# Kernel optimization log

Hardware: AMD Instinct MI355X
Metric: run time of the kernel (lower is better)

Reference implementation:

```python
import jax, jax.numpy as jnp
import numpy as np

N_NODES = 100000
N_EDGES = 1600000
N_FEAT = 128
N_HID = 128
N_CLASS = 10
N_GRAPHS = 512
BN_EPS = 1e-5


def setup_inputs() -> dict:
    key = jax.random.key(0)
    ks = jax.random.split(key, 12)
    x = jax.random.normal(ks[0], (N_NODES, N_FEAT), dtype=jnp.float32)
    edge_index = jax.random.randint(ks[1], (2, N_EDGES), 0, N_NODES, dtype=jnp.int32)
    batch = jnp.sort(jax.random.randint(ks[2], (N_NODES,), 0, N_GRAPHS, dtype=jnp.int32))
    s1 = 1.0 / np.sqrt(N_FEAT)
    s2 = 1.0 / np.sqrt(N_HID)
    W1 = jax.random.uniform(ks[3], (N_FEAT, N_HID), jnp.float32, -s1, s1)
    b1 = jax.random.uniform(ks[4], (N_HID,), jnp.float32, -s1, s1)
    gamma = jnp.ones((N_HID,), jnp.float32)
    beta = jnp.zeros((N_HID,), jnp.float32)
    W2 = jax.random.uniform(ks[5], (N_HID, N_HID), jnp.float32, -s2, s2)
    b2 = jax.random.uniform(ks[6], (N_HID,), jnp.float32, -s2, s2)
    clsW = jax.random.uniform(ks[7], (N_HID, N_CLASS), jnp.float32, -s2, s2)
    clsb = jax.random.uniform(ks[8], (N_CLASS,), jnp.float32, -s2, s2)
    return {"x": x, "edge_index": edge_index, "batch": batch,
            "W1": W1, "b1": b1, "gamma": gamma, "beta": beta,
            "W2": W2, "b2": b2, "clsW": clsW, "clsb": clsb}


def _gcn_norm(edge_index, n_nodes):
    # add self-loops, compute symmetric normalization D^-1/2 A_hat D^-1/2
    loops = jnp.arange(n_nodes, dtype=edge_index.dtype)
    src = jnp.concatenate([edge_index[0], loops])
    dst = jnp.concatenate([edge_index[1], loops])
    deg = jax.ops.segment_sum(jnp.ones_like(dst, dtype=jnp.float32), dst,
                              num_segments=n_nodes)
    dinv = jnp.where(deg > 0, jax.lax.rsqrt(deg), 0.0)
    norm = dinv[src] * dinv[dst]  # [E + N]
    return src, dst, norm


def _gcn_conv(h, src, dst, norm, W, b, n_nodes):
    h = h @ W                                   # [N, nhid] dense GEMM
    msg = h[src] * norm[:, None]                # gather + scale  [E+N, nhid]
    out = jax.ops.segment_sum(msg, dst, num_segments=n_nodes)  # scatter-add
    return out + b


def reference(x, edge_index, batch, W1, b1, gamma, beta, W2, b2, clsW, clsb):
    n_nodes = x.shape[0]
    src, dst, norm = _gcn_norm(edge_index, n_nodes)
    # layer 1: GCNConv -> BatchNorm(eval, running stats 0/1) -> ReLU -> Dropout(eval=id)
    h = _gcn_conv(x, src, dst, norm, W1, b1, n_nodes)
    h = h * (gamma / jnp.sqrt(1.0 + BN_EPS)) + beta
    h = jax.nn.relu(h)
    # layer 2: GCNConv (output layer, no bn/act)
    h = _gcn_conv(h, src, dst, norm, W2, b2, n_nodes)
    # global mean pool over batch index
    sums = jax.ops.segment_sum(h, batch, num_segments=N_GRAPHS)          # [G, nhid]
    cnts = jax.ops.segment_sum(jnp.ones((n_nodes,), h.dtype), batch,
                               num_segments=N_GRAPHS)
    g = sums / jnp.maximum(cnts, 1.0)[:, None]
    out = jax.nn.log_softmax(g @ clsW + clsb, axis=1)                    # [G, nclass]
    return out, g
```

## Files before the change

### kernel.cpp

```cpp
#include <hip/hip_runtime.h>
#include <hip/hip_bf16.h>

#define N_NODES 100000
#define N_EDGES 1600000
#define N_FEAT 128
#define N_HID 128
#define N_CLASS 10
#define N_GRAPHS 512
#define BN_RSQRT 0.9999950000374997f

#define NRANGE 12500
#define NSUB 512
#define SCAP 640
#define HGROUP 32
#define BPB (NSUB / HGROUP)

typedef _Float16 half_t;
typedef __attribute__((ext_vector_type(2))) _Float16 half2v;
typedef __attribute__((ext_vector_type(4))) _Float16 half4v;
typedef __attribute__((ext_vector_type(8))) _Float16 half8v;
typedef __attribute__((ext_vector_type(4))) float floatx4;
typedef __attribute__((ext_vector_type(2))) float floatx2;

__global__ __launch_bounds__(256) void bucket_fused(
    const int* __restrict__ src, const int* __restrict__ dst,
    int* __restrict__ cnt, unsigned long long* __restrict__ bucketed,
    const float* __restrict__ W1, half_t* __restrict__ Wt1,
    const float* __restrict__ W2, half_t* __restrict__ Wt2,
    const int* __restrict__ batch, int* __restrict__ boffs,
    int chunkE, int E, int nnodes)
{
    __shared__ int wcnt[4][8];
    __shared__ int wbase[4][8];
    int blk = blockIdx.x;
    if (blk >= NSUB) {
        int k = blk - NSUB;
        if (k < 128) {
            int i = k * 256 + threadIdx.x;
            const float* W = (i < 16384) ? W1 : W2;
            half_t* Wt = (i < 16384) ? Wt1 : Wt2;
            int j = i & 16383;
            int c = j >> 7, kk = j & 127;
            Wt[(size_t)c * 128 + kk] = (half_t)W[(size_t)kk * 128 + c];
        } else {
            int i = (k - 128) * 256 + threadIdx.x;
            if (i < nnodes) {
                int b = batch[i];
                int prev = (i == 0) ? -1 : batch[i - 1];
                for (int g = prev + 1; g <= b; ++g) boffs[g] = i;
                if (i == nnodes - 1)
                    for (int g = b + 1; g <= N_GRAPHS; ++g) boffs[g] = nnodes;
            }
        }
        return;
    }
    int b = blk;
    int wave = threadIdx.x >> 6;
    int lane = threadIdx.x & 63;
    int e0 = b * chunkE;
    int e1 = e0 + chunkE < E ? e0 + chunkE : E;
    int iters = (chunkE + 255) / 256;

    int mycnt = 0;
    for (int it = 0; it < iters; ++it) {
        int e = e0 + it * 256 + threadIdx.x;
        bool valid = e < e1;
        int d = valid ? dst[e] : 0;
        int rr = (d * 8) / N_NODES;
#pragma unroll
        for (int r = 0; r < 8; ++r) {
            unsigned long long m = __ballot(valid && rr == r);
            if (lane == r) mycnt += __popcll(m);
        }
    }
    if (lane < 8) wcnt[wave][lane] = mycnt;
    __syncthreads();
    if (threadIdx.x < 8) {
        int r = threadIdx.x;
        int s = 0;
#pragma unroll
        for (int w = 0; w < 4; ++w) { wbase[w][r] = s; s += wcnt[w][r]; }
        cnt[r * NSUB + b] = s;
    }
    __syncthreads();

    int myoff = (lane < 8) ? wbase[wave][lane] : 0;
    for (int it = 0; it < iters; ++it) {
        int e = e0 + it * 256 + threadIdx.x;
        bool valid = e < e1;
        int s = valid ? src[e] : 0;
        int d = valid ? dst[e] : 0;
        int rr = (d * 8) / N_NODES;
        unsigned long long pk = ((unsigned long long)(unsigned)d << 32) | (unsigned)s;
#pragma unroll
        for (int r = 0; r < 8; ++r) {
            unsigned long long m = __ballot(valid && rr == r);
            int base_r = __shfl(myoff, r);
            if (valid && rr == r) {
                int pos = base_r + __popcll(m & ((1ull << lane) - 1));
                if (pos < SCAP)
                    bucketed[(size_t)(r * NSUB + b) * SCAP + pos] = pk;
            }
            if (lane == r) myoff += __popcll(m);
        }
    }
}

__global__ __launch_bounds__(256) void hist2(
    const unsigned long long* __restrict__ bucketed, const int* __restrict__ cnt,
    int* __restrict__ partial)
{
    __shared__ int h[NRANGE];
    int r = blockIdx.x & 7, g = blockIdx.x >> 3;
    for (int i = threadIdx.x; i < NRANGE; i += 256) h[i] = 0;
    __syncthreads();
    int rbase = r * NRANGE;
    for (int j = 0; j < BPB; ++j) {
        int b = g * BPB + j;
        int n = cnt[r * NSUB + b];
        if (n > SCAP) n = SCAP;
        const unsigned long long* seg = bucketed + (size_t)(r * NSUB + b) * SCAP;
        for (int i = threadIdx.x; i < n; i += 256)
            atomicAdd(&h[(int)(seg[i] >> 32) - rbase], 1);
    }
    __syncthreads();
    int* slice = partial + (size_t)(r * HGROUP + g) * NRANGE;
    for (int i = threadIdx.x; i < NRANGE; i += 256) slice[i] = h[i];
}

__global__ void deg_reduce(const int* __restrict__ partial, int* __restrict__ deg,
                           float* __restrict__ dinv, int* __restrict__ bsums, int n) {
    __shared__ int sm[256];
    int t = threadIdx.x;
    int i = blockIdx.x * 256 + t;
    int s = 0;
    if (i < n) {
        int rr = i / NRANGE;
        int dl = i - rr * NRANGE;
        const int* p = partial + (size_t)rr * HGROUP * NRANGE + dl;
#pragma unroll 8
        for (int g = 0; g < HGROUP; ++g) s += p[(size_t)g * NRANGE];
        deg[i] = s;
        dinv[i] = rsqrtf((float)s + 1.0f);
    }
    sm[t] = s;
    __syncthreads();
    for (int off = 128; off > 0; off >>= 1) {
        if (t < off) sm[t] += sm[t + off];
        __syncthreads();
    }
    if (t == 0) bsums[blockIdx.x] = sm[0];
}

__global__ void scan_small(int* __restrict__ bsums, int nb) {
    __shared__ int buf[1024];
    int t = threadIdx.x;
    int v = (t < nb) ? bsums[t] : 0;
    buf[t] = v;
    __syncthreads();
    for (int off = 1; off < 1024; off <<= 1) {
        int x = (t >= off) ? buf[t - off] : 0;
        __syncthreads();
        buf[t] += x;
        __syncthreads();
    }
    if (t < nb) bsums[t] = buf[t] - v;
}

__global__ __launch_bounds__(256) void scan_chunkoff_gemm1(
    const int* __restrict__ in, const int* __restrict__ bsums,
    int* __restrict__ rowptr, int* __restrict__ partial,
    int n, int total, int nb,
    const float* __restrict__ X, const half_t* __restrict__ Wt,
    const float* __restrict__ dinv, unsigned char* __restrict__ Y8, int nrows)
{
    __shared__ int s[256];
    if (blockIdx.x < (unsigned)nb) {
        int t = threadIdx.x;
        int i = blockIdx.x * 256 + t;
        int v = (i < n) ? in[i] : 0;
        s[t] = v;
        __syncthreads();
        for (int off = 1; off < 256; off <<= 1) {
            int x = (t >= off) ? s[t - off] : 0;
            __syncthreads();
            s[t] += x;
            __syncthreads();
        }
        if (i == 0) rowptr[n] = total;
        if (i < n) {
            int excl = bsums[blockIdx.x] + s[t] - v;
            rowptr[i] = excl;
            int rr = i / NRANGE;
            int dl = i - rr * NRANGE;
            int* p = partial + (size_t)rr * HGROUP * NRANGE + dl;
            int running = excl;
            for (int g = 0; g < HGROUP; ++g) {
                int tmp = p[(size_t)g * NRANGE];
                p[(size_t)g * NRANGE] = running;
                running += tmp;
            }
        }
        return;
    }
    int bb = blockIdx.x - nb;
    int wave = threadIdx.x >> 6;
    int lane = threadIdx.x & 63;
    int n16  = lane & 15;
    int quad = lane >> 4;
    int r0 = bb * 64 + wave * 16;
    if (r0 >= nrows) return;
    int row = r0 + n16;
    const float4* xrow = (const float4*)(X + (size_t)row * 128);
    half8v a[4];
#pragma unroll
    for (int kc = 0; kc < 4; ++kc) {
        float4 f0 = xrow[kc * 8 + quad * 2];
        float4 f1 = xrow[kc * 8 + quad * 2 + 1];
        half8v t = {(half_t)f0.x, (half_t)f0.y, (half_t)f0.z, (half_t)f0.w,
                    (half_t)f1.x, (half_t)f1.y, (half_t)f1.z, (half_t)f1.w};
        a[kc] = t;
    }
    float dr = dinv[row];
#pragma unroll
    for (int c = 0; c < 8; ++c) {
        const half8v* wrow = (const half8v*)(Wt + (size_t)(c * 16 + n16) * 128);
        floatx4 acc = {0.f, 0.f, 0.f, 0.f};
        acc = __builtin_amdgcn_mfma_f32_16x16x32_f16(wrow[0 * 4 + quad], a[0], acc, 0, 0, 0);
        acc = __builtin_amdgcn_mfma_f32_16x16x32_f16(wrow[1 * 4 + quad], a[1], acc, 0, 0, 0);
        acc = __builtin_amdgcn_mfma_f32_16x16x32_f16(wrow[2 * 4 + quad], a[2], acc, 0, 0, 0);
        acc = __builtin_amdgcn_mfma_f32_16x16x32_f16(wrow[3 * 4 + quad], a[3], acc, 0, 0, 0);
        int packed = __builtin_amdgcn_cvt_pk_fp8_f32(acc[0] * dr, acc[1] * dr, 0, false);
        packed = __builtin_amdgcn_cvt_pk_fp8_f32(acc[2] * dr, acc[3] * dr, packed, true);
        *(int*)(Y8 + (size_t)row * 128 + c * 16 + quad * 4) = packed;
    }
}

__global__ __launch_bounds__(256) void fill2(
    const unsigned long long* __restrict__ bucketed, const int* __restrict__ cnt,
    const int* __restrict__ partial, int* __restrict__ col)
{
    __shared__ int off[NRANGE];
    int r = blockIdx.x & 7, g = blockIdx.x >> 3;
    const int* slice = partial + (size_t)(r * HGROUP + g) * NRANGE;
    for (int i = threadIdx.x; i < NRANGE; i += 256) off[i] = slice[i];
    __syncthreads();
    int rbase = r * NRANGE;
    for (int j = 0; j < BPB; ++j) {
        int b = g * BPB + j;
        int n = cnt[r * NSUB + b];
        if (n > SCAP) n = SCAP;
        const unsigned long long* seg = bucketed + (size_t)(r * NSUB + b) * SCAP;
        for (int i = threadIdx.x; i < n; i += 256) {
            unsigned long long pk = seg[i];
            int pos = atomicAdd(&off[(int)(pk >> 32) - rbase], 1);
            col[pos] = (int)((unsigned)(pk & 0xffffffffu) << 7);
        }
    }
}

__global__ __launch_bounds__(256) void gemm2_mfma(
    const half_t* __restrict__ X, const half_t* __restrict__ Wt,
    const float* __restrict__ dinv, unsigned char* __restrict__ Y8, int nrows)
{
    int wave = threadIdx.x >> 6;
    int lane = threadIdx.x & 63;
    int n16  = lane & 15;
    int quad = lane >> 4;
    int r0 = blockIdx.x * 64 + wave * 16;
    if (r0 >= nrows) return;
    int row = r0 + n16;
    const half8v* xrow = (const half8v*)(X + (size_t)row * 128);
    half8v a0 = xrow[0 * 4 + quad];
    half8v a1 = xrow[1 * 4 + quad];
    half8v a2 = xrow[2 * 4 + quad];
    half8v a3 = xrow[3 * 4 + quad];
    float dr = dinv[row];
#pragma unroll
    for (int c = 0; c < 8; ++c) {
        const half8v* wrow = (const half8v*)(Wt + (size_t)(c * 16 + n16) * 128);
        floatx4 acc = {0.f, 0.f, 0.f, 0.f};
        acc = __builtin_amdgcn_mfma_f32_16x16x32_f16(wrow[0 * 4 + quad], a0, acc, 0, 0, 0);
        acc = __builtin_amdgcn_mfma_f32_16x16x32_f16(wrow[1 * 4 + quad], a1, acc, 0, 0, 0);
        acc = __builtin_amdgcn_mfma_f32_16x16x32_f16(wrow[2 * 4 + quad], a2, acc, 0, 0, 0);
        acc = __builtin_amdgcn_mfma_f32_16x16x32_f16(wrow[3 * 4 + quad], a3, acc, 0, 0, 0);
        int packed = __builtin_amdgcn_cvt_pk_fp8_f32(acc[0] * dr, acc[1] * dr, 0, false);
        packed = __builtin_amdgcn_cvt_pk_fp8_f32(acc[2] * dr, acc[3] * dr, packed, true);
        *(int*)(Y8 + (size_t)row * 128 + c * 16 + quad * 4) = packed;
    }
}

__global__ __launch_bounds__(256) void agg_fp8(
    const unsigned char* __restrict__ hs, half_t* __restrict__ out,
    const int* __restrict__ col, const int* __restrict__ rowptr,
    const float* __restrict__ dinv, const float* __restrict__ bias,
    const float* __restrict__ gamma, const float* __restrict__ beta,
    int nnodes, int do_bn_relu)
{
    int wave = threadIdx.x >> 6;
    int lane = threadIdx.x & 63;
    int i = blockIdx.x * 4 + wave;
    if (i >= nnodes) return;
    int hf = lane >> 5;
    unsigned f4 = (unsigned)(lane & 31) << 2;
    unsigned ZOFF = (unsigned)nnodes << 7;
    int e0 = rowptr[i], e1 = rowptr[i + 1];
    floatx2 a01 = {0.f, 0.f}, a23 = {0.f, 0.f};
    floatx2 b01 = {0.f, 0.f}, b23 = {0.f, 0.f};
    for (int base = e0; base < e1; base += 64) {
        int idx = base + lane;
        unsigned ecol = (idx < e1) ? (unsigned)col[idx] : ZOFF;
        int lim = base + 64 < e1 ? base + 64 : e1;
        for (int e = base; e < lim; e += 16) {
            int j = e - base + hf;
            unsigned s0 = __shfl(ecol, j + 0);
            unsigned s1 = __shfl(ecol, j + 2);
            unsigned s2 = __shfl(ecol, j + 4);
            unsigned s3 = __shfl(ecol, j + 6);
            unsigned s4 = __shfl(ecol, j + 8);
            unsigned s5 = __shfl(ecol, j + 10);
            unsigned s6 = __shfl(ecol, j + 12);
            unsigned s7 = __shfl(ecol, j + 14);
            unsigned v0 = *(const unsigned*)(hs + (s0 | f4));
            unsigned v1 = *(const unsigned*)(hs + (s1 | f4));
            unsigned v2 = *(const unsigned*)(hs + (s2 | f4));
            unsigned v3 = *(const unsigned*)(hs + (s3 | f4));
            unsigned v4 = *(const unsigned*)(hs + (s4 | f4));
            unsigned v5 = *(const unsigned*)(hs + (s5 | f4));
            unsigned v6 = *(const unsigned*)(hs + (s6 | f4));
            unsigned v7 = *(const unsigned*)(hs + (s7 | f4));
            a01 += __builtin_amdgcn_cvt_pk_f32_fp8((int)v0, false);
            a23 += __builtin_amdgcn_cvt_pk_f32_fp8((int)v0, true);
            b01 += __builtin_amdgcn_cvt_pk_f32_fp8((int)v1, false);
            b23 += __builtin_amdgcn_cvt_pk_f32_fp8((int)v1, true);
            a01 += __builtin_amdgcn_cvt_pk_f32_fp8((int)v2, false);
            a23 += __builtin_amdgcn_cvt_pk_f32_fp8((int)v2, true);
            b01 += __builtin_amdgcn_cvt_pk_f32_fp8((int)v3, false);
            b23 += __builtin_amdgcn_cvt_pk_f32_fp8((int)v3, true);
            a01 += __builtin_amdgcn_cvt_pk_f32_fp8((int)v4, false);
            a23 += __builtin_amdgcn_cvt_pk_f32_fp8((int)v4, true);
            b01 += __builtin_amdgcn_cvt_pk_f32_fp8((int)v5, false);
            b23 += __builtin_amdgcn_cvt_pk_f32_fp8((int)v5, true);
            a01 += __builtin_amdgcn_cvt_pk_f32_fp8((int)v6, false);
            a23 += __builtin_amdgcn_cvt_pk_f32_fp8((int)v6, true);
            b01 += __builtin_amdgcn_cvt_pk_f32_fp8((int)v7, false);
            b23 += __builtin_amdgcn_cvt_pk_f32_fp8((int)v7, true);
        }
    }
    a01 += b01;
    a23 += b23;
    float c0 = a01.x + __shfl_xor(a01.x, 32);
    float c1 = a01.y + __shfl_xor(a01.y, 32);
    float c2 = a23.x + __shfl_xor(a23.x, 32);
    float c3 = a23.y + __shfl_xor(a23.y, 32);
    if (hf == 0) {
        unsigned vs = *(const unsigned*)(hs + (((unsigned)i << 7) | f4));
        floatx2 fs01 = __builtin_amdgcn_cvt_pk_f32_fp8((int)vs, false);
        floatx2 fs23 = __builtin_amdgcn_cvt_pk_f32_fp8((int)vs, true);
        float di = dinv[i];
        float4 bi = *(const float4*)(bias + f4);
        float o0 = di * (c0 + fs01.x) + bi.x;
        float o1 = di * (c1 + fs01.y) + bi.y;
        float o2 = di * (c2 + fs23.x) + bi.z;
        float o3 = di * (c3 + fs23.y) + bi.w;
        if (do_bn_relu) {
            float4 ga = *(const float4*)(gamma + f4);
            float4 be = *(const float4*)(beta + f4);
            o0 = fmaf(o0, ga.x * BN_RSQRT, be.x);
            o1 = fmaf(o1, ga.y * BN_RSQRT, be.y);
            o2 = fmaf(o2, ga.z * BN_RSQRT, be.z);
            o3 = fmaf(o3, ga.w * BN_RSQRT, be.w);
            o0 = o0 > 0.f ? o0 : 0.f;
            o1 = o1 > 0.f ? o1 : 0.f;
            o2 = o2 > 0.f ? o2 : 0.f;
            o3 = o3 > 0.f ? o3 : 0.f;
        }
        half4v ov = {(half_t)o0, (half_t)o1, (half_t)o2, (half_t)o3};
        *(half4v*)(out + (size_t)i * 128 + f4) = ov;
    }
}

__global__ __launch_bounds__(512) void pool_cls(
    const half_t* __restrict__ h, const int* __restrict__ boffs,
    const float* __restrict__ clsW, const float* __restrict__ clsb,
    float* __restrict__ gout, float* __restrict__ out)
{
    __shared__ float red[8][128];
    __shared__ float zbuf[16];
    int g = blockIdx.x;
    int w = threadIdx.x >> 6;
    int lane = threadIdx.x & 63;
    int n0 = boffs[g], n1 = boffs[g + 1];
    float ax = 0.f, ay = 0.f;
    for (int n = n0 + w; n < n1; n += 8) {
        half2v v = *(const half2v*)(h + (size_t)n * 128 + lane * 2);
        ax += (float)v.x;
        ay += (float)v.y;
    }
    red[w][lane * 2] = ax;
    red[w][lane * 2 + 1] = ay;
    __syncthreads();
    if (w == 0) {
        float sx = 0.f, sy = 0.f;
#pragma unroll
        for (int j = 0; j < 8; ++j) {
            sx += red[j][lane * 2];
            sy += red[j][lane * 2 + 1];
        }
        float cnt = (float)((n1 - n0) > 1 ? (n1 - n0) : 1);
        float g0 = sx / cnt, g1 = sy / cnt;
        gout[(size_t)g * 128 + lane * 2] = g0;
        gout[(size_t)g * 128 + lane * 2 + 1] = g1;
        red[0][lane * 2] = g0;
        red[0][lane * 2 + 1] = g1;
    }
    __syncthreads();
    if (threadIdx.x < N_CLASS) {
        int c = threadIdx.x;
        float z = clsb[c];
        for (int k = 0; k < N_HID; ++k)
            z = fmaf(red[0][k], clsW[k * N_CLASS + c], z);
        zbuf[c] = z;
    }
    __syncthreads();
    if (threadIdx.x == 0) {
        float m = zbuf[0];
#pragma unroll
        for (int c = 1; c < N_CLASS; ++c) m = fmaxf(m, zbuf[c]);
        float s = 0.f;
#pragma unroll
        for (int c = 0; c < N_CLASS; ++c) s += expf(zbuf[c] - m);
        float l = logf(s);
#pragma unroll
        for (int c = 0; c < N_CLASS; ++c)
            out[(size_t)g * N_CLASS + c] = zbuf[c] - m - l;
    }
}

extern "C" void kernel_launch(void* const* d_in, const int* in_sizes, int n_in,
                              void* d_out, int out_size, void* d_ws, size_t ws_size,
                              hipStream_t stream) {
    const float* x     = (const float*)d_in[0];
    const int*   ei    = (const int*)d_in[1];
    const int*   batch = (const int*)d_in[2];
    const float* W1    = (const float*)d_in[3];
    const float* b1    = (const float*)d_in[4];
    const float* gamma = (const float*)d_in[5];
    const float* beta  = (const float*)d_in[6];
    const float* W2    = (const float*)d_in[7];
    const float* b2    = (const float*)d_in[8];
    const float* clsW  = (const float*)d_in[9];
    const float* clsb  = (const float*)d_in[10];

    const int N = in_sizes[0] / N_FEAT;
    const int E = in_sizes[1] / 2;
    const int* src = ei;
    const int* dst = ei + E;

    unsigned char* BA8 = (unsigned char*)d_ws;
    half_t* BB = (half_t*)(BA8 + (size_t)(N + 1) * 128);
    half_t* Wt1 = BB + (size_t)N * 128;
    half_t* Wt2 = Wt1 + 16384;
    int*   col     = (int*)(Wt2 + 16384);
    int*   rowptr  = col + E;
    int*   deg     = rowptr + (N + 4);
    float* dinv    = (float*)(deg + N);
    int*   cnt     = (int*)(dinv + N);
    unsigned long long* bucketed =
        (unsigned long long*)(cnt + 8 * NSUB);
    int*   partial = (int*)(bucketed + (size_t)8 * NSUB * SCAP);
    int*   boffs   = partial + 8 * HGROUP * NRANGE;
    int*   bsums   = boffs + N_GRAPHS + 4;

    const int nb = (N + 255) / 256;
    const int chunkE = (E + NSUB - 1) / NSUB;
    const int gemmBlocks = (N + 63) / 64;

    hipMemsetAsync(BA8 + (size_t)N * 128, 0, 128, stream);

    bucket_fused<<<NSUB + 128 + nb, 256, 0, stream>>>(
        src, dst, cnt, bucketed, W1, Wt1, W2, Wt2, batch, boffs, chunkE, E, N);
    hist2<<<8 * HGROUP, 256, 0, stream>>>(bucketed, cnt, partial);
    deg_reduce<<<nb, 256, 0, stream>>>(partial, deg, dinv, bsums, N);
    scan_small<<<1, 1024, 0, stream>>>(bsums, nb);
    scan_chunkoff_gemm1<<<nb + gemmBlocks, 256, 0, stream>>>(
        deg, bsums, rowptr, partial, N, E, nb, x, Wt1, dinv, BA8, N);
    fill2<<<256, 256, 0, stream>>>(bucketed, cnt, partial, col);
    agg_fp8<<<(N + 3) / 4, 256, 0, stream>>>(BA8, BB, col, rowptr, dinv, b1, gamma, beta, N, 1);
    gemm2_mfma<<<gemmBlocks, 256, 0, stream>>>(BB, Wt2, dinv, BA8, N);
    agg_fp8<<<(N + 3) / 4, 256, 0, stream>>>(BA8, BB, col, rowptr, dinv, b2, gamma, beta, N, 0);

    float* out = (float*)d_out;
    float* gsec = out + (size_t)N_GRAPHS * N_CLASS;
    pool_cls<<<N_GRAPHS, 512, 0, stream>>>(BB, boffs, clsW, clsb, gsec, out);
}
```

Measured before the change: 331.8 us.

## Make aggregation kernel persistent with prefetch of next node's edge list

Converts the per-node aggregation kernel into a fixed-size grid-stride loop in which each wave prefetches the row pointers and column indices of its next nodes while gathering the current one. Bias, gamma and beta loads are hoisted out of the loop, and the dinv lookup is replaced by computing rsqrt of the row degree plus one. This aims to hide index-load latency and cut per-node launch overhead, but it reduces how many waves are available to hide gather latency.

```diff
diff --git a/kernel.cpp b/kernel.cpp
--- a/kernel.cpp
+++ b/kernel.cpp
@@ -290,93 +290,124 @@
     }
 }
 
+#define AGG16(CV, BASE_E)                                                     \
+    {                                                                         \
+        int j = (BASE_E) + hf;                                                \
+        unsigned s0 = __shfl(CV, j + 0);                                      \
+        unsigned s1 = __shfl(CV, j + 2);                                      \
+        unsigned s2 = __shfl(CV, j + 4);                                      \
+        unsigned s3 = __shfl(CV, j + 6);                                      \
+        unsigned s4 = __shfl(CV, j + 8);                                      \
+        unsigned s5 = __shfl(CV, j + 10);                                     \
+        unsigned s6 = __shfl(CV, j + 12);                                     \
+        unsigned s7 = __shfl(CV, j + 14);                                     \
+        unsigned v0 = *(const unsigned*)(hs + (s0 | f4));                     \
+        unsigned v1 = *(const unsigned*)(hs + (s1 | f4));                     \
+        unsigned v2 = *(const unsigned*)(hs + (s2 | f4));                     \
+        unsigned v3 = *(const unsigned*)(hs + (s3 | f4));                     \
+        unsigned v4 = *(const unsigned*)(hs + (s4 | f4));                     \
+        unsigned v5 = *(const unsigned*)(hs + (s5 | f4));                     \
+        unsigned v6 = *(const unsigned*)(hs + (s6 | f4));                     \
+        unsigned v7 = *(const unsigned*)(hs + (s7 | f4));                     \
+        a01 += __builtin_amdgcn_cvt_pk_f32_fp8((int)v0, false);               \
+        a23 += __builtin_amdgcn_cvt_pk_f32_fp8((int)v0, true);                \
+        b01 += __builtin_amdgcn_cvt_pk_f32_fp8((int)v1, false);               \
+        b23 += __builtin_amdgcn_cvt_pk_f32_fp8((int)v1, true);                \
+        a01 += __builtin_amdgcn_cvt_pk_f32_fp8((int)v2, false);               \
+        a23 += __builtin_amdgcn_cvt_pk_f32_fp8((int)v2, true);                \
+        b01 += __builtin_amdgcn_cvt_pk_f32_fp8((int)v3, false);               \
+        b23 += __builtin_amdgcn_cvt_pk_f32_fp8((int)v3, true);                \
+        a01 += __builtin_amdgcn_cvt_pk_f32_fp8((int)v4, false);               \
+        a23 += __builtin_amdgcn_cvt_pk_f32_fp8((int)v4, true);                \
+        b01 += __builtin_amdgcn_cvt_pk_f32_fp8((int)v5, false);               \
+        b23 += __builtin_amdgcn_cvt_pk_f32_fp8((int)v5, true);                \
+        a01 += __builtin_amdgcn_cvt_pk_f32_fp8((int)v6, false);               \
+        a23 += __builtin_amdgcn_cvt_pk_f32_fp8((int)v6, true);                \
+        b01 += __builtin_amdgcn_cvt_pk_f32_fp8((int)v7, false);               \
+        b23 += __builtin_amdgcn_cvt_pk_f32_fp8((int)v7, true);                \
+    }
+
 __global__ __launch_bounds__(256) void agg_fp8(
     const unsigned char* __restrict__ hs, half_t* __restrict__ out,
     const int* __restrict__ col, const int* __restrict__ rowptr,
-    const float* __restrict__ dinv, const float* __restrict__ bias,
+    const float* __restrict__ bias,
     const float* __restrict__ gamma, const float* __restrict__ beta,
     int nnodes, int do_bn_relu)
 {
     int wave = threadIdx.x >> 6;
     int lane = threadIdx.x & 63;
-    int i = blockIdx.x * 4 + wave;
-    if (i >= nnodes) return;
+    int wid = blockIdx.x * 4 + wave;
+    int W = gridDim.x * 4;
     int hf = lane >> 5;
     unsigned f4 = (unsigned)(lane & 31) << 2;
     unsigned ZOFF = (unsigned)nnodes << 7;
+
+    float4 bi = *(const float4*)(bias + f4);
+    float4 ga = *(const float4*)(gamma + f4);
+    float4 be = *(const float4*)(beta + f4);
+
+    int i = wid;
+    if (i >= nnodes) return;
     int e0 = rowptr[i], e1 = rowptr[i + 1];
-    floatx2 a01 = {0.f, 0.f}, a23 = {0.f, 0.f};
-    floatx2 b01 = {0.f, 0.f}, b23 = {0.f, 0.f};
-    for (int base = e0; base < e1; base += 64) {
-        int idx = base + lane;
-        unsigned ecol = (idx < e1) ? (unsigned)col[idx] : ZOFF;
-        int lim = base + 64 < e1 ? base + 64 : e1;
-        for (int e = base; e < lim; e += 16) {
-            int j = e - base + hf;
-            unsigned s0 = __shfl(ecol, j + 0);
-            unsigned s1 = __shfl(ecol, j + 2);
-            unsigned s2 = __shfl(ecol, j + 4);
-            unsigned s3 = __shfl(ecol, j + 6);
-            unsigned s4 = __shfl(ecol, j + 8);
-            unsigned s5 = __shfl(ecol, j + 10);
-            unsigned s6 = __shfl(ecol, j + 12);
-            unsigned s7 = __shfl(ecol, j + 14);
-            unsigned v0 = *(const unsigned*)(hs + (s0 | f4));
-            unsigned v1 = *(const unsigned*)(hs + (s1 | f4));
-            unsigned v2 = *(const unsigned*)(hs + (s2 | f4));
-            unsigned v3 = *(const unsigned*)(hs + (s3 | f4));
-            unsigned v4 = *(const unsigned*)(hs + (s4 | f4));
-            unsigned v5 = *(const unsigned*)(hs + (s5 | f4));
-            unsigned v6 = *(const unsigned*)(hs + (s6 | f4));
-            unsigned v7 = *(const unsigned*)(hs + (s7 | f4));
-            a01 += __builtin_amdgcn_cvt_pk_f32_fp8((int)v0, false);
-            a23 += __builtin_amdgcn_cvt_pk_f32_fp8((int)v0, true);
-            b01 += __builtin_amdgcn_cvt_pk_f32_fp8((int)v1, false);
-            b23 += __builtin_amdgcn_cvt_pk_f32_fp8((int)v1, true);
-            a01 += __builtin_amdgcn_cvt_pk_f32_fp8((int)v2, false);
-            a23 += __builtin_amdgcn_cvt_pk_f32_fp8((int)v2, true);
-            b01 += __builtin_amdgcn_cvt_pk_f32_fp8((int)v3, false);
-            b23 += __builtin_amdgcn_cvt_pk_f32_fp8((int)v3, true);
-            a01 += __builtin_amdgcn_cvt_pk_f32_fp8((int)v4, false);
-            a23 += __builtin_amdgcn_cvt_pk_f32_fp8((int)v4, true);
-            b01 += __builtin_amdgcn_cvt_pk_f32_fp8((int)v5, false);
-            b23 += __builtin_amdgcn_cvt_pk_f32_fp8((int)v5, true);
-            a01 += __builtin_amdgcn_cvt_pk_f32_fp8((int)v6, false);
-            a23 += __builtin_amdgcn_cvt_pk_f32_fp8((int)v6, true);
-            b01 += __builtin_amdgcn_cvt_pk_f32_fp8((int)v7, false);
-            b23 += __builtin_amdgcn_cvt_pk_f32_fp8((int)v7, true);
-        }
-    }
-    a01 += b01;
-    a23 += b23;
-    float c0 = a01.x + __shfl_xor(a01.x, 32);
-    float c1 = a01.y + __shfl_xor(a01.y, 32);
-    float c2 = a23.x + __shfl_xor(a23.x, 32);
-    float c3 = a23.y + __shfl_xor(a23.y, 32);
-    if (hf == 0) {
+    int i2 = i + W;
+    int e0n = 0, e1n = 0;
+    if (i2 < nnodes) { e0n = rowptr[i2]; e1n = rowptr[i2 + 1]; }
+    int idx = e0 + lane;
+    unsigned colv = (idx < e1) ? (unsigned)col[idx] : ZOFF;
+
+    for (;;) {
+        unsigned colvn = ZOFF;
+        if (i2 < nnodes) {
+            int idxn = e0n + lane;
+            if (idxn < e1n) colvn = (unsigned)col[idxn];
+        }
+        int i3 = i2 + W;
+        int e0nn = 0, e1nn = 0;
+        if (i3 < nnodes) { e0nn = rowptr[i3]; e1nn = rowptr[i3 + 1]; }
         unsigned vs = *(const unsigned*)(hs + (((unsigned)i << 7) | f4));
-        floatx2 fs01 = __builtin_amdgcn_cvt_pk_f32_fp8((int)vs, false);
-        floatx2 fs23 = __builtin_amdgcn_cvt_pk_f32_fp8((int)vs, true);
-        float di = dinv[i];
-        float4 bi = *(const float4*)(bias + f4);
-        float o0 = di * (c0 + fs01.x) + bi.x;
-        float o1 = di * (c1 + fs01.y) + bi.y;
-        float o2 = di * (c2 + fs23.x) + bi.z;
-        float o3 = di * (c3 + fs23.y) + bi.w;
-        if (do_bn_relu) {
-            float4 ga = *(const float4*)(gamma + f4);
-            float4 be = *(const float4*)(beta + f4);
-            o0 = fmaf(o0, ga.x * BN_RSQRT, be.x);
-            o1 = fmaf(o1, ga.y * BN_RSQRT, be.y);
-            o2 = fmaf(o2, ga.z * BN_RSQRT, be.z);
-            o3 = fmaf(o3, ga.w * BN_RSQRT, be.w);
-            o0 = o0 > 0.f ? o0 : 0.f;
-            o1 = o1 > 0.f ? o1 : 0.f;
-            o2 = o2 > 0.f ? o2 : 0.f;
-            o3 = o3 > 0.f ? o3 : 0.f;
-        }
-        half4v ov = {(half_t)o0, (half_t)o1, (half_t)o2, (half_t)o3};
-        *(half4v*)(out + (size_t)i * 128 + f4) = ov;
+
+        floatx2 a01 = {0.f, 0.f}, a23 = {0.f, 0.f};
+        floatx2 b01 = {0.f, 0.f}, b23 = {0.f, 0.f};
+        int lim0 = e0 + 64 < e1 ? e0 + 64 : e1;
+        for (int e = e0; e < lim0; e += 16) AGG16(colv, e - e0)
+        for (int base = e0 + 64; base < e1; base += 64) {
+            int idx2 = base + lane;
+            unsigned ecol = (idx2 < e1) ? (unsigned)col[idx2] : ZOFF;
+            int lim = base + 64 < e1 ? base + 64 : e1;
+            for (int e = base; e < lim; e += 16) AGG16(ecol, e - base)
+        }
+
+        a01 += b01;
+        a23 += b23;
+        float c0 = a01.x + __shfl_xor(a01.x, 32);
+        float c1 = a01.y + __shfl_xor(a01.y, 32);
+        float c2 = a23.x + __shfl_xor(a23.x, 32);
+        float c3 = a23.y + __shfl_xor(a23.y, 32);
+        if (hf == 0) {
+            floatx2 fs01 = __builtin_amdgcn_cvt_pk_f32_fp8((int)vs, false);
+            floatx2 fs23 = __builtin_amdgcn_cvt_pk_f32_fp8((int)vs, true);
+            float di = rsqrtf((float)(e1 - e0) + 1.0f);
+            float o0 = di * (c0 + fs01.x) + bi.x;
+            float o1 = di * (c1 + fs01.y) + bi.y;
+            float o2 = di * (c2 + fs23.x) + bi.z;
+            float o3 = di * (c3 + fs23.y) + bi.w;
+            if (do_bn_relu) {
+                o0 = fmaf(o0, ga.x * BN_RSQRT, be.x);
+                o1 = fmaf(o1, ga.y * BN_RSQRT, be.y);
+                o2 = fmaf(o2, ga.z * BN_RSQRT, be.z);
+                o3 = fmaf(o3, ga.w * BN_RSQRT, be.w);
+                o0 = o0 > 0.f ? o0 : 0.f;
+                o1 = o1 > 0.f ? o1 : 0.f;
+                o2 = o2 > 0.f ? o2 : 0.f;
+                o3 = o3 > 0.f ? o3 : 0.f;
+            }
+            half4v ov = {(half_t)o0, (half_t)o1, (half_t)o2, (half_t)o3};
+            *(half4v*)(out + (size_t)i * 128 + f4) = ov;
+        }
+
+        if (i2 >= nnodes) break;
+        i = i2; e0 = e0n; e1 = e1n; colv = colvn;
+        i2 = i3; e0n = e0nn; e1n = e1nn;
     }
 }
 
@@ -475,6 +506,7 @@
     const int nb = (N + 255) / 256;
     const int chunkE = (E + NSUB - 1) / NSUB;
     const int gemmBlocks = (N + 63) / 64;
+    const int aggBlocks = 2048;
 
     hipMemsetAsync(BA8 + (size_t)N * 128, 0, 128, stream);
 
@@ -486,9 +518,9 @@
     scan_chunkoff_gemm1<<<nb + gemmBlocks, 256, 0, stream>>>(
         deg, bsums, rowptr, partial, N, E, nb, x, Wt1, dinv, BA8, N);
     fill2<<<256, 256, 0, stream>>>(bucketed, cnt, partial, col);
-    agg_fp8<<<(N + 3) / 4, 256, 0, stream>>>(BA8, BB, col, rowptr, dinv, b1, gamma, beta, N, 1);
+    agg_fp8<<<aggBlocks, 256, 0, stream>>>(BA8, BB, col, rowptr, b1, gamma, beta, N, 1);
     gemm2_mfma<<<gemmBlocks, 256, 0, stream>>>(BB, Wt2, dinv, BA8, N);
-    agg_fp8<<<(N + 3) / 4, 256, 0, stream>>>(BA8, BB, col, rowptr, dinv, b2, gamma, beta, N, 0);
+    agg_fp8<<<aggBlocks, 256, 0, stream>>>(BA8, BB, col, rowptr, b2, gamma, beta, N, 0);
 
     float* out = (float*)d_out;
     float* gsec = out + (size_t)N_GRAPHS * N_CLASS;
```

Result: no change. 335.5 us (+1.1%).

## Restructure fp8 aggregation to full-wave rows with scalar-broadcast edge indices

Applied to the files above, without the earlier changes.

The aggregation kernel now has every one of the 64 lanes own two features of the row, instead of two half-waves each splitting the edge list over four features. Neighbor indices are broadcast with readlane in chunks of 16 edges, which removes the cross-half shuffle reduction. The self-loop load is issued early, and dinv is recomputed from the rowptr difference rather than loaded. This trades fewer shuffles and a shorter tail for narrower 2-byte gathers and more load instructions per edge.

```diff
diff --git a/kernel.cpp b/kernel.cpp
--- a/kernel.cpp
+++ b/kernel.cpp
@@ -293,7 +293,7 @@
 __global__ __launch_bounds__(256) void agg_fp8(
     const unsigned char* __restrict__ hs, half_t* __restrict__ out,
     const int* __restrict__ col, const int* __restrict__ rowptr,
-    const float* __restrict__ dinv, const float* __restrict__ bias,
+    const float* __restrict__ bias,
     const float* __restrict__ gamma, const float* __restrict__ beta,
     int nnodes, int do_bn_relu)
 {
@@ -301,83 +301,45 @@
     int lane = threadIdx.x & 63;
     int i = blockIdx.x * 4 + wave;
     if (i >= nnodes) return;
-    int hf = lane >> 5;
-    unsigned f4 = (unsigned)(lane & 31) << 2;
+    unsigned f2 = (unsigned)lane << 1;
     unsigned ZOFF = (unsigned)nnodes << 7;
-    int e0 = rowptr[i], e1 = rowptr[i + 1];
-    floatx2 a01 = {0.f, 0.f}, a23 = {0.f, 0.f};
-    floatx2 b01 = {0.f, 0.f}, b23 = {0.f, 0.f};
-    for (int base = e0; base < e1; base += 64) {
-        int idx = base + lane;
-        unsigned ecol = (idx < e1) ? (unsigned)col[idx] : ZOFF;
-        int lim = base + 64 < e1 ? base + 64 : e1;
-        for (int e = base; e < lim; e += 16) {
-            int j = e - base + hf;
-            unsigned s0 = __shfl(ecol, j + 0);
-            unsigned s1 = __shfl(ecol, j + 2);
-            unsigned s2 = __shfl(ecol, j + 4);
-            unsigned s3 = __shfl(ecol, j + 6);
-            unsigned s4 = __shfl(ecol, j + 8);
-            unsigned s5 = __shfl(ecol, j + 10);
-            unsigned s6 = __shfl(ecol, j + 12);
-            unsigned s7 = __shfl(ecol, j + 14);
-            unsigned v0 = *(const unsigned*)(hs + (s0 | f4));
-            unsigned v1 = *(const unsigned*)(hs + (s1 | f4));
-            unsigned v2 = *(const unsigned*)(hs + (s2 | f4));
-            unsigned v3 = *(const unsigned*)(hs + (s3 | f4));
-            unsigned v4 = *(const unsigned*)(hs + (s4 | f4));
-            unsigned v5 = *(const unsigned*)(hs + (s5 | f4));
-            unsigned v6 = *(const unsigned*)(hs + (s6 | f4));
-            unsigned v7 = *(const unsigned*)(hs + (s7 | f4));
-            a01 += __builtin_amdgcn_cvt_pk_f32_fp8((int)v0, false);
-            a23 += __builtin_amdgcn_cvt_pk_f32_fp8((int)v0, true);
-            b01 += __builtin_amdgcn_cvt_pk_f32_fp8((int)v1, false);
-            b23 += __builtin_amdgcn_cvt_pk_f32_fp8((int)v1, true);
-            a01 += __builtin_amdgcn_cvt_pk_f32_fp8((int)v2, false);
-            a23 += __builtin_amdgcn_cvt_pk_f32_fp8((int)v2, true);
-            b01 += __builtin_amdgcn_cvt_pk_f32_fp8((int)v3, false);
-            b23 += __builtin_amdgcn_cvt_pk_f32_fp8((int)v3, true);
-            a01 += __builtin_amdgcn_cvt_pk_f32_fp8((int)v4, false);
-            a23 += __builtin_amdgcn_cvt_pk_f32_fp8((int)v4, true);
-            b01 += __builtin_amdgcn_cvt_pk_f32_fp8((int)v5, false);
-            b23 += __builtin_amdgcn_cvt_pk_f32_fp8((int)v5, true);
-            a01 += __builtin_amdgcn_cvt_pk_f32_fp8((int)v6, false);
-            a23 += __builtin_amdgcn_cvt_pk_f32_fp8((int)v6, true);
-            b01 += __builtin_amdgcn_cvt_pk_f32_fp8((int)v7, false);
-            b23 += __builtin_amdgcn_cvt_pk_f32_fp8((int)v7, true);
-        }
-    }
-    a01 += b01;
-    a23 += b23;
-    float c0 = a01.x + __shfl_xor(a01.x, 32);
-    float c1 = a01.y + __shfl_xor(a01.y, 32);
-    float c2 = a23.x + __shfl_xor(a23.x, 32);
-    float c3 = a23.y + __shfl_xor(a23.y, 32);
-    if (hf == 0) {
-        unsigned vs = *(const unsigned*)(hs + (((unsigned)i << 7) | f4));
-        floatx2 fs01 = __builtin_amdgcn_cvt_pk_f32_fp8((int)vs, false);
-        floatx2 fs23 = __builtin_amdgcn_cvt_pk_f32_fp8((int)vs, true);
-        float di = dinv[i];
-        float4 bi = *(const float4*)(bias + f4);
-        float o0 = di * (c0 + fs01.x) + bi.x;
-        float o1 = di * (c1 + fs01.y) + bi.y;
-        float o2 = di * (c2 + fs23.x) + bi.z;
-        float o3 = di * (c3 + fs23.y) + bi.w;
-        if (do_bn_relu) {
-            float4 ga = *(const float4*)(gamma + f4);
-            float4 be = *(const float4*)(beta + f4);
-            o0 = fmaf(o0, ga.x * BN_RSQRT, be.x);
-            o1 = fmaf(o1, ga.y * BN_RSQRT, be.y);
-            o2 = fmaf(o2, ga.z * BN_RSQRT, be.z);
-            o3 = fmaf(o3, ga.w * BN_RSQRT, be.w);
-            o0 = o0 > 0.f ? o0 : 0.f;
-            o1 = o1 > 0.f ? o1 : 0.f;
-            o2 = o2 > 0.f ? o2 : 0.f;
-            o3 = o3 > 0.f ? o3 : 0.f;
-        }
-        half4v ov = {(half_t)o0, (half_t)o1, (half_t)o2, (half_t)o3};
-        *(half4v*)(out + (size_t)i * 128 + f4) = ov;
-    }
+
+    int e0 = __builtin_amdgcn_readfirstlane(rowptr[i]);
+    int e1 = __builtin_amdgcn_readfirstlane(rowptr[i + 1]);
+
+    unsigned short us = *(const unsigned short*)(hs + (((unsigned)i << 7) | f2));
+
+    floatx2 acc0 = {0.f, 0.f}, acc1 = {0.f, 0.f};
+    for (int base = e0; base < e1; base += 16) {
+        int idx = base + (lane & 15);
+        unsigned cv = (idx < e1) ? (unsigned)col[idx] : ZOFF;
+#pragma unroll
+        for (int k = 0; k < 16; k += 2) {
+            unsigned sa = (unsigned)__builtin_amdgcn_readlane((int)cv, k);
+            unsigned sb = (unsigned)__builtin_amdgcn_readlane((int)cv, k + 1);
+            unsigned short ua = *(const unsigned short*)(hs + (sa | f2));
+            unsigned short ub = *(const unsigned short*)(hs + (sb | f2));
+            acc0 += __builtin_amdgcn_cvt_pk_f32_fp8((int)(unsigned)ua, false);
+            acc1 += __builtin_amdgcn_cvt_pk_f32_fp8((int)(unsigned)ub, false);
+        }
+    }
+    floatx2 acc = acc0 + acc1;
+    acc += __builtin_amdgcn_cvt_pk_f32_fp8((int)(unsigned)us, false);
+
+    float di = rsqrtf((float)(e1 - e0) + 1.0f);
+    float2 bi = *(const float2*)(bias + 2 * lane);
+    float o0 = fmaf(di, acc.x, bi.x);
+    float o1 = fmaf(di, acc.y, bi.y);
+    if (do_bn_relu) {
+        float2 ga = *(const float2*)(gamma + 2 * lane);
+        float2 be = *(const float2*)(beta + 2 * lane);
+        o0 = fmaf(o0, ga.x * BN_RSQRT, be.x);
+        o1 = fmaf(o1, ga.y * BN_RSQRT, be.y);
+        o0 = o0 > 0.f ? o0 : 0.f;
+        o1 = o1 > 0.f ? o1 : 0.f;
+    }
+    half2v ov = {(half_t)o0, (half_t)o1};
+    *(half2v*)(out + (size_t)i * 128 + 2 * lane) = ov;
 }
 
 __global__ __launch_bounds__(512) void pool_cls(
@@ -486,9 +448,9 @@
     scan_chunkoff_gemm1<<<nb + gemmBlocks, 256, 0, stream>>>(
         deg, bsums, rowptr, partial, N, E, nb, x, Wt1, dinv, BA8, N);
     fill2<<<256, 256, 0, stream>>>(bucketed, cnt, partial, col);
-    agg_fp8<<<(N + 3) / 4, 256, 0, stream>>>(BA8, BB, col, rowptr, dinv, b1, gamma, beta, N, 1);
+    agg_fp8<<<(N + 3) / 4, 256, 0, stream>>>(BA8, BB, col, rowptr, b1, gamma, beta, N, 1);
     gemm2_mfma<<<gemmBlocks, 256, 0, stream>>>(BB, Wt2, dinv, BA8, N);
-    agg_fp8<<<(N + 3) / 4, 256, 0, stream>>>(BA8, BB, col, rowptr, dinv, b2, gamma, beta, N, 0);
+    agg_fp8<<<(N + 3) / 4, 256, 0, stream>>>(BA8, BB, col, rowptr, b2, gamma, beta, N, 0);
 
     float* out = (float*)d_out;
     float* gsec = out + (size_t)N_GRAPHS * N_CLASS;
```

After: 329.9 us. About the same (-0.6%).
